# Performance work log

Hardware: AMD Instinct MI355X
Metric: run time of the kernel (lower is better)

The kernel has to match this reference:

```python
import jax, jax.numpy as jnp
import numpy as np

N_HEADS = 2

def setup_inputs() -> dict:
    key = jax.random.key(0)
    ks = jax.random.split(key, 10)
    d, bank, b, t = 192, 1000, 16, 4096
    s = 1.0 / np.sqrt(d)
    return {
        "z": jax.random.normal(ks[0], (b, d, t), jnp.float32),
        "memory_bank": jax.random.normal(ks[1], (d, bank), jnp.float32),
        "Wq": jax.random.normal(ks[2], (d, d), jnp.float32) * s,
        "bq": jax.random.normal(ks[3], (d,), jnp.float32) * 0.02,
        "Wk": jax.random.normal(ks[4], (d, d), jnp.float32) * s,
        "bk": jax.random.normal(ks[5], (d,), jnp.float32) * 0.02,
        "Wv": jax.random.normal(ks[6], (d, d), jnp.float32) * s,
        "bv": jax.random.normal(ks[7], (d,), jnp.float32) * 0.02,
        "Wo": jax.random.normal(ks[8], (d, d), jnp.float32) * s,
        "bo": jax.random.normal(ks[9], (d,), jnp.float32) * 0.02,
    }


def _split_heads(x):
    # x: [b, d, t] -> [b, h, t, dk]  (matches view(b, h, dk, t).transpose(2, 3))
    b, d, t = x.shape
    dk = d // N_HEADS
    return x.reshape(b, N_HEADS, dk, t).transpose(0, 1, 3, 2)


def reference(z, memory_bank, Wq, bq, Wk, bk, Wv, bv, Wo, bo):
    b, d, t = z.shape
    dk = d // N_HEADS
    # memory bank expanded over batch: [b, d, bank]
    c = jnp.broadcast_to(memory_bank[None], (b,) + memory_bank.shape)
    # 1x1 conv projections == per-channel linear
    q = jnp.einsum('oc,bct->bot', Wq, z) + bq[None, :, None]
    k = jnp.einsum('oc,bcs->bos', Wk, c) + bk[None, :, None]
    v = jnp.einsum('oc,bcs->bos', Wv, c) + bv[None, :, None]
    qh = _split_heads(q)  # [b, h, t, dk]
    kh = _split_heads(k)  # [b, h, bank, dk]
    vh = _split_heads(v)  # [b, h, bank, dk]
    scores = jnp.einsum('bhtd,bhsd->bhts', qh, kh) / jnp.sqrt(jnp.asarray(dk, z.dtype))
    p = jax.nn.softmax(scores, axis=-1)  # [b, h, t, bank]
    out = jnp.einsum('bhts,bhsd->bhtd', p, vh)  # [b, h, t, dk]
    out = out.transpose(0, 1, 3, 2).reshape(b, d, t)  # merge heads -> [b, d, t]
    return jnp.einsum('oc,bct->bot', Wo, out) + bo[None, :, None]
```

## Files before the change

kernel.cpp:

```cpp
#include <hip/hip_runtime.h>


typedef float  f32x4  __attribute__((ext_vector_type(4)));
typedef __bf16 bf16;
typedef __bf16 bf16x8 __attribute__((ext_vector_type(8)));

#define B_   16
#define D_   192
#define T_   4096
#define BANK 1000
#define SP   1024
#define DK   96
#define SCALE 0.10206207261596577f
#define LOG2E 1.4426950408889634f

__global__ __launch_bounds__(256) void kv_kernel(
    const float* __restrict__ mb, const float* __restrict__ Wk, const float* __restrict__ bk,
    const float* __restrict__ Wv, const float* __restrict__ bv,
    bf16* __restrict__ ktg, bf16* __restrict__ vtg) {
  int s = blockIdx.x * 256 + threadIdx.x;
  int o = blockIdx.y;
  int h = o / DK, i = o % DK;
  float ak = 0.f, av = 0.f;
  if (s < BANK) {
    ak = bk[o]; av = bv[o];
    for (int c = 0; c < D_; ++c) {
      float m = mb[c * BANK + s];
      ak += Wk[o * D_ + c] * m;
      av += Wv[o * D_ + c] * m;
    }
  }
  ktg[(size_t)(h * SP + s) * DK + i] = (bf16)ak;
  vtg[(size_t)(h * DK + i) * SP + s] = (bf16)av;
}

__global__ __launch_bounds__(256) void zt_kernel(const float* __restrict__ z,
                                                 bf16* __restrict__ zT) {
  __shared__ __align__(16) bf16 sT[64 * 200];
  const int tid = threadIdx.x;
  const int t0 = blockIdx.x * 64, b = blockIdx.y;
#pragma unroll
  for (int it = 0; it < 48; ++it) {
    int e = tid + 256 * it;
    int c = e >> 6, tl = e & 63;
    sT[tl * 200 + c] = (bf16)z[((size_t)b * D_ + c) * T_ + t0 + tl];
  }
  __syncthreads();
#pragma unroll
  for (int it = 0; it < 6; ++it) {
    int g = tid + 256 * it;
    int tl = g / 24, c8 = (g % 24) * 8;
    bf16x8 v = *(const bf16x8*)&sT[tl * 200 + c8];
    *(bf16x8*)&zT[((size_t)b * T_ + t0 + tl) * D_ + c8] = v;
  }
}

__global__ __launch_bounds__(256) void proj_kernel(
    const bf16* __restrict__ XT, const float* __restrict__ W,
    const float* __restrict__ bias, float* __restrict__ Y, float outscale) {
  __shared__ __align__(16) char smem[40960];
  bf16* sA = (bf16*)smem;
  bf16* sB = (bf16*)(smem + 16384);
  float* sE = (float*)smem;

  const int tid = threadIdx.x;
  const int t0 = blockIdx.x * 256, o0 = blockIdx.y * 64, b = blockIdx.z;
  const int lane = tid & 63, wv = tid >> 6;
  const int quad = lane >> 4, l15 = lane & 15;

#pragma unroll
  for (int r = 0; r < 6; ++r) {
    int g = tid + 256 * r;
    int kb = g >> 8, nt = (g >> 6) & 3, qd = (g >> 4) & 3, l5 = g & 15;
    const float* wp = &W[(o0 + nt * 16 + l5) * D_ + kb * 32 + qd * 8];
    f32x4 wa = *(const f32x4*)wp, wb = *(const f32x4*)(wp + 4);
    bf16x8 pk;
#pragma unroll
    for (int u = 0; u < 4; ++u) { pk[u] = (bf16)wa[u]; pk[4 + u] = (bf16)wb[u]; }
    *(bf16x8*)&sB[(size_t)g * 8] = pk;
  }

  f32x4 acc[4][4];
#pragma unroll
  for (int m = 0; m < 4; ++m)
#pragma unroll
    for (int n = 0; n < 4; ++n) acc[m][n] = (f32x4){0.f, 0.f, 0.f, 0.f};

  for (int kb = 0; kb < 6; ++kb) {
    __syncthreads();
#pragma unroll
    for (int r = 0; r < 4; ++r) {
      int g = tid + 256 * r;
      int tg = g >> 6, qd = (g >> 4) & 3, l5 = g & 15;
      bf16x8 v = *(const bf16x8*)&XT[((size_t)b * T_ + t0 + tg * 16 + l5) * D_ +
                                     kb * 32 + qd * 8];
      *(bf16x8*)&sA[(size_t)g * 8] = v;
    }
    __syncthreads();
    bf16x8 bf[4];
#pragma unroll
    for (int n = 0; n < 4; ++n)
      bf[n] = *(const bf16x8*)&sB[(size_t)((kb * 4 + n) * 64 + lane) * 8];
#pragma unroll
    for (int m = 0; m < 4; ++m) {
      bf16x8 af = *(const bf16x8*)&sA[(size_t)((wv * 4 + m) * 64 + lane) * 8];
#pragma unroll
      for (int n = 0; n < 4; ++n)
        acc[m][n] = __builtin_amdgcn_mfma_f32_16x16x32_bf16(af, bf[n], acc[m][n], 0, 0, 0);
    }
  }
  __syncthreads();

  float bs[4];
#pragma unroll
  for (int n = 0; n < 4; ++n) bs[n] = bias[o0 + n * 16 + l15];
  float* se = sE + wv * 1088;
#pragma unroll
  for (int m = 0; m < 4; ++m) {
#pragma unroll
    for (int n = 0; n < 4; ++n)
#pragma unroll
      for (int r = 0; r < 4; ++r)
        se[(quad * 4 + r) * 68 + n * 16 + l15] = (acc[m][n][r] + bs[n]) * outscale;
#pragma unroll
    for (int oo = 0; oo < 16; ++oo) {
      int ol = oo * 4 + quad;
      Y[((size_t)b * D_ + o0 + ol) * T_ + t0 + wv * 64 + m * 16 + l15] =
          se[l15 * 68 + ol];
    }
  }
}

__global__ __launch_bounds__(256, 4) void attn_kernel(
    const float* __restrict__ qws, const bf16* __restrict__ ktg,
    const bf16* __restrict__ vtg, bf16* __restrict__ owsT) {
  __shared__ __align__(16) char smem[28672];
  bf16* kt = (bf16*)smem;
  bf16* vt = (bf16*)(smem + 12288);
  bf16* sP = (bf16*)(smem + 24576);
  bf16* qt = (bf16*)smem;
  float* sO = (float*)smem;

  const int tid = threadIdx.x;
  const int t0 = blockIdx.x * 64, h = blockIdx.y, b = blockIdx.z;
  const int lane = tid & 63, wv = tid >> 6;
  const int quad = lane >> 4, l15 = lane & 15;

  const bf16* kb_g = ktg + (size_t)h * SP * DK;
  const bf16* vb_g = vtg + (size_t)h * DK * SP;

  const bf16* kp[3];
  const bf16* vp[3];
#pragma unroll
  for (int r = 0; r < 3; ++r) {
    int g = tid + 256 * r;
    {
      int kb = g >> 8, n = (g >> 6) & 3, qd = (g >> 4) & 3, l5 = g & 15;
      kp[r] = kb_g + (size_t)(n * 16 + l5) * DK + kb * 32 + qd * 8;
    }
    {
      int gg = g >> 6;
      int kb = gg / 6, n = gg % 6, qd = (g >> 4) & 3, l5 = g & 15;
      vp[r] = vb_g + (size_t)(n * 16 + l5) * SP + kb * 32 + qd * 8;
    }
  }

  bf16x8 kreg[3], vreg[3];
#pragma unroll
  for (int r = 0; r < 3; ++r) {
    kreg[r] = *(const bf16x8*)kp[r];
    vreg[r] = *(const bf16x8*)vp[r];
  }

#pragma unroll
  for (int r = 0; r < 24; ++r) {
    int idx = tid + 256 * r;
    int i = idx >> 6, t = idx & 63;
    float v = qws[((size_t)(b * D_ + h * DK + i)) * T_ + t0 + t];
    int kb = i >> 5, qd = (i >> 3) & 3, j = i & 7, w = t >> 4, l5 = t & 15;
    qt[(size_t)(((kb * 4 + w) * 64 + qd * 16 + l5)) * 8 + j] = (bf16)v;
  }
  __syncthreads();
  bf16x8 qf[3];
#pragma unroll
  for (int kb = 0; kb < 3; ++kb)
    qf[kb] = *(const bf16x8*)&qt[(size_t)((kb * 4 + wv) * 64 + lane) * 8];

  f32x4 oacc[6];
#pragma unroll
  for (int n = 0; n < 6; ++n) oacc[n] = (f32x4){0.f, 0.f, 0.f, 0.f};
  float m_run[4] = {-1e30f, -1e30f, -1e30f, -1e30f};
  float l_run[4] = {0.f, 0.f, 0.f, 0.f};

  for (int ch = 0; ch < 16; ++ch) {
    __syncthreads();
#pragma unroll
    for (int r = 0; r < 3; ++r) {
      *(bf16x8*)&kt[(size_t)(tid + 256 * r) * 8] = kreg[r];
      *(bf16x8*)&vt[(size_t)(tid + 256 * r) * 8] = vreg[r];
    }
    __syncthreads();
    if (ch < 15) {
      const size_t ko = (size_t)(ch + 1) * 64 * DK;
      const size_t vo = (size_t)(ch + 1) * 64;
#pragma unroll
      for (int r = 0; r < 3; ++r) {
        kreg[r] = *(const bf16x8*)(kp[r] + ko);
        vreg[r] = *(const bf16x8*)(vp[r] + vo);
      }
    }

    f32x4 sacc[4];
#pragma unroll
    for (int n = 0; n < 4; ++n) sacc[n] = (f32x4){0.f, 0.f, 0.f, 0.f};
#pragma unroll
    for (int kb = 0; kb < 3; ++kb) {
#pragma unroll
      for (int n = 0; n < 4; ++n) {
        bf16x8 bfm = *(const bf16x8*)&kt[(size_t)((kb * 4 + n) * 64 + lane) * 8];
        sacc[n] = __builtin_amdgcn_mfma_f32_16x16x32_bf16(qf[kb], bfm, sacc[n], 0, 0, 0);
      }
    }
    if (ch == 15) {
#pragma unroll
      for (int r = 0; r < 4; ++r) {
        if (l15 >= 8) sacc[2][r] = -1e30f;
        sacc[3][r] = -1e30f;
      }
    }

    float mc[4];
#pragma unroll
    for (int r = 0; r < 4; ++r) {
      float m0 = fmaxf(fmaxf(sacc[0][r], sacc[1][r]), fmaxf(sacc[2][r], sacc[3][r]));
      m0 = fmaxf(m0, __shfl_xor(m0, 1, 64));
      m0 = fmaxf(m0, __shfl_xor(m0, 2, 64));
      m0 = fmaxf(m0, __shfl_xor(m0, 4, 64));
      m0 = fmaxf(m0, __shfl_xor(m0, 8, 64));
      mc[r] = m0;
    }
    bool keep = (mc[0] - m_run[0] <= 8.f) && (mc[1] - m_run[1] <= 8.f) &&
                (mc[2] - m_run[2] <= 8.f) && (mc[3] - m_run[3] <= 8.f);
    if (!__all(keep)) {
#pragma unroll
      for (int r = 0; r < 4; ++r) {
        float mn = fmaxf(m_run[r], mc[r]);
        float al = exp2f(m_run[r] - mn);
        m_run[r] = mn;
        l_run[r] *= al;
#pragma unroll
        for (int n = 0; n < 6; ++n) oacc[n][r] *= al;
      }
    }
    float pr[4][4];
#pragma unroll
    for (int r = 0; r < 4; ++r) {
      float ls = 0.f;
#pragma unroll
      for (int n = 0; n < 4; ++n) { pr[n][r] = exp2f(sacc[n][r] - m_run[r]); ls += pr[n][r]; }
      ls += __shfl_xor(ls, 1, 64);
      ls += __shfl_xor(ls, 2, 64);
      ls += __shfl_xor(ls, 4, 64);
      ls += __shfl_xor(ls, 8, 64);
      l_run[r] += ls;
    }

#pragma unroll
    for (int kb = 0; kb < 2; ++kb) {
#pragma unroll
      for (int nn = 0; nn < 2; ++nn) {
        int n = kb * 2 + nn;
        int qd2 = (nn << 1) | (l15 >> 3), j = l15 & 7;
#pragma unroll
        for (int r = 0; r < 4; ++r)
          sP[(size_t)((wv * 64 + qd2 * 16 + quad * 4 + r)) * 8 + j] = (bf16)pr[n][r];
      }
      bf16x8 pa = *(const bf16x8*)&sP[(size_t)(wv * 64 + lane) * 8];
#pragma unroll
      for (int n2 = 0; n2 < 6; ++n2) {
        bf16x8 vf = *(const bf16x8*)&vt[(size_t)((kb * 6 + n2) * 64 + lane) * 8];
        oacc[n2] = __builtin_amdgcn_mfma_f32_16x16x32_bf16(pa, vf, oacc[n2], 0, 0, 0);
      }
    }
  }

  float inv[4];
#pragma unroll
  for (int r = 0; r < 4; ++r) inv[r] = 1.0f / l_run[r];
  __syncthreads();
#pragma unroll
  for (int n = 0; n < 6; ++n)
#pragma unroll
    for (int r = 0; r < 4; ++r)
      sO[(n * 16 + l15) * 68 + wv * 16 + quad * 4 + r] = oacc[n][r] * inv[r];
  __syncthreads();
#pragma unroll
  for (int r = 0; r < 24; ++r) {
    int idx = tid + 256 * r;
    int t = idx / 96, i = idx % 96;
    owsT[((size_t)b * T_ + t0 + t) * D_ + h * DK + i] = (bf16)sO[i * 68 + t];
  }
}

extern "C" void kernel_launch(void* const* d_in, const int* in_sizes, int n_in,
                              void* d_out, int out_size, void* d_ws, size_t ws_size,
                              hipStream_t stream) {
  const float* z  = (const float*)d_in[0];
  const float* mb = (const float*)d_in[1];
  const float* Wq = (const float*)d_in[2];
  const float* bq = (const float*)d_in[3];
  const float* Wk = (const float*)d_in[4];
  const float* bk = (const float*)d_in[5];
  const float* Wv = (const float*)d_in[6];
  const float* bv = (const float*)d_in[7];
  const float* Wo = (const float*)d_in[8];
  const float* bo = (const float*)d_in[9];
  float* out = (float*)d_out;

  bf16* ktg  = (bf16*)d_ws;
  bf16* vtg  = ktg + 2 * SP * DK;
  bf16* zT   = vtg + 2 * DK * SP;
  bf16* owsT = zT + (size_t)B_ * T_ * D_;
  float* qws = (float*)(owsT + (size_t)B_ * T_ * D_);

  kv_kernel  <<<dim3(SP / 256, D_),    256, 0, stream>>>(mb, Wk, bk, Wv, bv, ktg, vtg);
  zt_kernel  <<<dim3(T_ / 64, B_),     256, 0, stream>>>(z, zT);
  proj_kernel<<<dim3(T_ / 256, 3, B_), 256, 0, stream>>>(zT, Wq, bq, qws, SCALE * LOG2E);
  attn_kernel<<<dim3(T_ / 64, 2, B_),  256, 0, stream>>>(qws, ktg, vtg, owsT);
  proj_kernel<<<dim3(T_ / 256, 3, B_), 256, 0, stream>>>(owsT, Wo, bo, out, 1.0f);
}
```

Baseline: 300.8 us.

## Store Q in bf16, double attention tile to 128 rows with 512 threads

The Q projection now writes bf16 instead of fp32, which halves the Q write and read traffic and lets the attention kernel load Q with 8-wide vector loads. The attention block grows to 512 threads covering 128 query rows, so each staged K/V chunk is shared by twice as many waves. The load work is split so that each thread stages either K or V. The P scratch store is swizzled to reduce LDS bank conflicts, and the output transpose is done per wave in bf16 without a block-wide barrier. The trade-off is fewer blocks with more registers and LDS per block, which may lower occupancy.

```diff
diff --git a/kernel.cpp b/kernel.cpp
--- a/kernel.cpp
+++ b/kernel.cpp
@@ -55,9 +55,10 @@
   }
 }
 
+template <typename OT>
 __global__ __launch_bounds__(256) void proj_kernel(
     const bf16* __restrict__ XT, const float* __restrict__ W,
-    const float* __restrict__ bias, float* __restrict__ Y, float outscale) {
+    const float* __restrict__ bias, OT* __restrict__ Y, float outscale) {
   __shared__ __align__(16) char smem[40960];
   bf16* sA = (bf16*)smem;
   bf16* sB = (bf16*)(smem + 16384);
@@ -126,65 +127,65 @@
     for (int oo = 0; oo < 16; ++oo) {
       int ol = oo * 4 + quad;
       Y[((size_t)b * D_ + o0 + ol) * T_ + t0 + wv * 64 + m * 16 + l15] =
-          se[l15 * 68 + ol];
-    }
-  }
-}
-
-__global__ __launch_bounds__(256, 4) void attn_kernel(
-    const float* __restrict__ qws, const bf16* __restrict__ ktg,
+          (OT)se[l15 * 68 + ol];
+    }
+  }
+}
+
+__global__ __launch_bounds__(512) void attn_kernel(
+    const bf16* __restrict__ qws, const bf16* __restrict__ ktg,
     const bf16* __restrict__ vtg, bf16* __restrict__ owsT) {
-  __shared__ __align__(16) char smem[28672];
+  __shared__ __align__(16) char smem[32768];
   bf16* kt = (bf16*)smem;
   bf16* vt = (bf16*)(smem + 12288);
   bf16* sP = (bf16*)(smem + 24576);
   bf16* qt = (bf16*)smem;
-  float* sO = (float*)smem;
 
   const int tid = threadIdx.x;
-  const int t0 = blockIdx.x * 64, h = blockIdx.y, b = blockIdx.z;
+  const int t0 = blockIdx.x * 128, h = blockIdx.y, b = blockIdx.z;
   const int lane = tid & 63, wv = tid >> 6;
   const int quad = lane >> 4, l15 = lane & 15;
 
   const bf16* kb_g = ktg + (size_t)h * SP * DK;
   const bf16* vb_g = vtg + (size_t)h * DK * SP;
 
-  const bf16* kp[3];
-  const bf16* vp[3];
+  const bf16* sp_ptr[3];
+  int sp_str[3];
 #pragma unroll
   for (int r = 0; r < 3; ++r) {
-    int g = tid + 256 * r;
-    {
+    int g = tid + 512 * r;
+    if (g < 768) {
       int kb = g >> 8, n = (g >> 6) & 3, qd = (g >> 4) & 3, l5 = g & 15;
-      kp[r] = kb_g + (size_t)(n * 16 + l5) * DK + kb * 32 + qd * 8;
-    }
-    {
-      int gg = g >> 6;
-      int kb = gg / 6, n = gg % 6, qd = (g >> 4) & 3, l5 = g & 15;
-      vp[r] = vb_g + (size_t)(n * 16 + l5) * SP + kb * 32 + qd * 8;
-    }
-  }
-
-  bf16x8 kreg[3], vreg[3];
+      sp_ptr[r] = kb_g + (size_t)(n * 16 + l5) * DK + kb * 32 + qd * 8;
+      sp_str[r] = 64 * DK;
+    } else {
+      int gv = g - 768, blk = gv >> 6;
+      int kbv = blk / 6, n = blk % 6, qd = (gv >> 4) & 3, l5 = gv & 15;
+      sp_ptr[r] = vb_g + (size_t)(n * 16 + l5) * SP + kbv * 32 + qd * 8;
+      sp_str[r] = 64;
+    }
+  }
+  bf16x8 kreg[3];
+#pragma unroll
+  for (int r = 0; r < 3; ++r) kreg[r] = *(const bf16x8*)sp_ptr[r];
+
 #pragma unroll
   for (int r = 0; r < 3; ++r) {
-    kreg[r] = *(const bf16x8*)kp[r];
-    vreg[r] = *(const bf16x8*)vp[r];
-  }
-
-#pragma unroll
-  for (int r = 0; r < 24; ++r) {
-    int idx = tid + 256 * r;
-    int i = idx >> 6, t = idx & 63;
-    float v = qws[((size_t)(b * D_ + h * DK + i)) * T_ + t0 + t];
-    int kb = i >> 5, qd = (i >> 3) & 3, j = i & 7, w = t >> 4, l5 = t & 15;
-    qt[(size_t)(((kb * 4 + w) * 64 + qd * 16 + l5)) * 8 + j] = (bf16)v;
+    int g8 = tid + 512 * r;
+    int i = g8 >> 4, t8 = (g8 & 15) * 8;
+    bf16x8 v = *(const bf16x8*)&qws[((size_t)(b * D_ + h * DK + i)) * T_ + t0 + t8];
+    int kb = i >> 5, qd = (i >> 3) & 3, j = i & 7;
+#pragma unroll
+    for (int tt = 0; tt < 8; ++tt) {
+      int t = t8 + tt;
+      qt[(size_t)((kb * 8 + (t >> 4)) * 64 + qd * 16 + (t & 15)) * 8 + j] = v[tt];
+    }
   }
   __syncthreads();
   bf16x8 qf[3];
 #pragma unroll
   for (int kb = 0; kb < 3; ++kb)
-    qf[kb] = *(const bf16x8*)&qt[(size_t)((kb * 4 + wv) * 64 + lane) * 8];
+    qf[kb] = *(const bf16x8*)&qt[(size_t)((kb * 8 + wv) * 64 + lane) * 8];
 
   f32x4 oacc[6];
 #pragma unroll
@@ -195,18 +196,14 @@
   for (int ch = 0; ch < 16; ++ch) {
     __syncthreads();
 #pragma unroll
-    for (int r = 0; r < 3; ++r) {
-      *(bf16x8*)&kt[(size_t)(tid + 256 * r) * 8] = kreg[r];
-      *(bf16x8*)&vt[(size_t)(tid + 256 * r) * 8] = vreg[r];
-    }
+    for (int r = 0; r < 3; ++r)
+      *(bf16x8*)(smem + (size_t)(tid + 512 * r) * 16) = kreg[r];
     __syncthreads();
     if (ch < 15) {
-      const size_t ko = (size_t)(ch + 1) * 64 * DK;
-      const size_t vo = (size_t)(ch + 1) * 64;
 #pragma unroll
       for (int r = 0; r < 3; ++r) {
-        kreg[r] = *(const bf16x8*)(kp[r] + ko);
-        vreg[r] = *(const bf16x8*)(vp[r] + vo);
+        sp_ptr[r] += sp_str[r];
+        kreg[r] = *(const bf16x8*)sp_ptr[r];
       }
     }
 
@@ -273,9 +270,10 @@
         int qd2 = (nn << 1) | (l15 >> 3), j = l15 & 7;
 #pragma unroll
         for (int r = 0; r < 4; ++r)
-          sP[(size_t)((wv * 64 + qd2 * 16 + quad * 4 + r)) * 8 + j] = (bf16)pr[n][r];
-      }
-      bf16x8 pa = *(const bf16x8*)&sP[(size_t)(wv * 64 + lane) * 8];
+          sP[(size_t)(wv * 64 + qd2 * 16 + quad * 4 + (r ^ quad)) * 8 + j] =
+              (bf16)pr[n][r];
+      }
+      bf16x8 pa = *(const bf16x8*)&sP[(size_t)(wv * 64 + (lane ^ ((lane >> 2) & 3))) * 8];
 #pragma unroll
       for (int n2 = 0; n2 < 6; ++n2) {
         bf16x8 vf = *(const bf16x8*)&vt[(size_t)((kb * 6 + n2) * 64 + lane) * 8];
@@ -288,17 +286,17 @@
 #pragma unroll
   for (int r = 0; r < 4; ++r) inv[r] = 1.0f / l_run[r];
   __syncthreads();
-#pragma unroll
-  for (int n = 0; n < 6; ++n)
+  bf16* sOw = (bf16*)smem + wv * (96 * 17);
+#pragma unroll
+  for (int n2 = 0; n2 < 6; ++n2)
 #pragma unroll
     for (int r = 0; r < 4; ++r)
-      sO[(n * 16 + l15) * 68 + wv * 16 + quad * 4 + r] = oacc[n][r] * inv[r];
-  __syncthreads();
-#pragma unroll
-  for (int r = 0; r < 24; ++r) {
-    int idx = tid + 256 * r;
-    int t = idx / 96, i = idx % 96;
-    owsT[((size_t)b * T_ + t0 + t) * D_ + h * DK + i] = (bf16)sO[i * 68 + t];
+      sOw[(n2 * 16 + l15) * 17 + quad * 4 + r] = (bf16)(oacc[n2][r] * inv[r]);
+#pragma unroll
+  for (int r2 = 0; r2 < 24; ++r2) {
+    int g = r2 * 64 + lane;
+    int tl = g / 96, i = g % 96;
+    owsT[((size_t)b * T_ + t0 + wv * 16 + tl) * D_ + h * DK + i] = sOw[i * 17 + tl];
   }
 }
 
@@ -321,11 +319,11 @@
   bf16* vtg  = ktg + 2 * SP * DK;
   bf16* zT   = vtg + 2 * DK * SP;
   bf16* owsT = zT + (size_t)B_ * T_ * D_;
-  float* qws = (float*)(owsT + (size_t)B_ * T_ * D_);
-
-  kv_kernel  <<<dim3(SP / 256, D_),    256, 0, stream>>>(mb, Wk, bk, Wv, bv, ktg, vtg);
-  zt_kernel  <<<dim3(T_ / 64, B_),     256, 0, stream>>>(z, zT);
-  proj_kernel<<<dim3(T_ / 256, 3, B_), 256, 0, stream>>>(zT, Wq, bq, qws, SCALE * LOG2E);
-  attn_kernel<<<dim3(T_ / 64, 2, B_),  256, 0, stream>>>(qws, ktg, vtg, owsT);
-  proj_kernel<<<dim3(T_ / 256, 3, B_), 256, 0, stream>>>(owsT, Wo, bo, out, 1.0f);
-}
+  bf16* qws  = owsT + (size_t)B_ * T_ * D_;
+
+  kv_kernel        <<<dim3(SP / 256, D_),    256, 0, stream>>>(mb, Wk, bk, Wv, bv, ktg, vtg);
+  zt_kernel        <<<dim3(T_ / 64, B_),     256, 0, stream>>>(z, zT);
+  proj_kernel<bf16><<<dim3(T_ / 256, 3, B_), 256, 0, stream>>>(zT, Wq, bq, qws, SCALE * LOG2E);
+  attn_kernel      <<<dim3(T_ / 128, 2, B_), 512, 0, stream>>>(qws, ktg, vtg, owsT);
+  proj_kernel<float><<<dim3(T_ / 256, 3, B_), 256, 0, stream>>>(owsT, Wo, bo, out, 1.0f);
+}
```

After: 300.0 us. Within noise of the previous version (-0.2%).
